# Performance work log

Hardware: AMD Instinct MI355X
Metric: run time of the kernel (lower is better)

The kernel has to match this reference:

```python
import jax, jax.numpy as jnp
import numpy as np

B, N, X, Y, W1, W2, D = 2, 6, 8, 8, 8, 8, 128
H, DH = 4, 32
L = X * Y          # number of windows
QT = N * W1 * W2   # tokens per window
EPS = 1e-5


def _ln(x, g, b):
    m = x.mean(-1, keepdims=True)
    v = ((x - m) ** 2).mean(-1, keepdims=True)
    return (x - m) * jax.lax.rsqrt(v + EPS) * g + b


def _win(t):
    # b n x y w1 w2 d -> b (x y) (n w1 w2) d
    return t.transpose(0, 2, 3, 1, 4, 5, 6).reshape(B, L, QT, D)


def setup_inputs() -> dict:
    key = jax.random.key(0)
    ks = jax.random.split(key, 12)
    s = 0.02
    inp = {
        'q': jax.random.normal(ks[0], (B, N, X, Y, W1, W2, D), jnp.float32),
        'k': jax.random.normal(ks[1], (B, N, X, Y, W1, W2, D), jnp.float32),
        'v': jax.random.normal(ks[2], (B, N, X, Y, W1, W2, D), jnp.float32),
        'skip': jax.random.normal(ks[3], (B, X, Y, W1, W2, D), jnp.float32),
        'gq': jnp.ones((D,), jnp.float32), 'betq': jnp.zeros((D,), jnp.float32),
        'gk': jnp.ones((D,), jnp.float32), 'betk': jnp.zeros((D,), jnp.float32),
        'gv': jnp.ones((D,), jnp.float32), 'betv': jnp.zeros((D,), jnp.float32),
        'wq': jax.random.normal(ks[4], (D, H * DH), jnp.float32) * s,
        'bq': jnp.zeros((H * DH,), jnp.float32),
        'wk': jax.random.normal(ks[5], (D, H * DH), jnp.float32) * s,
        'bk': jnp.zeros((H * DH,), jnp.float32),
        'wv': jax.random.normal(ks[6], (D, H * DH), jnp.float32) * s,
        'bv': jnp.zeros((H * DH,), jnp.float32),
        'wp': jax.random.normal(ks[7], (H * DH, D), jnp.float32) * s,
        'bp': jnp.zeros((D,), jnp.float32),
    }
    return inp


def reference(q, k, v, skip, gq, betq, gk, betk, gv, betv,
              wq, bq, wk, bk, wv, bv, wp, bp):
    scale = DH ** -0.5
    qw, kw, vw = _win(q), _win(k), _win(v)
    # LayerNorm + Linear QKV, split heads: (b, l, T, h, dh)
    qh = (_ln(qw, gq, betq) @ wq + bq).reshape(B, L, QT, H, DH)
    kh = (_ln(kw, gk, betk) @ wk + bk).reshape(B, L, QT, H, DH)
    vh = (_ln(vw, gv, betv) @ wv + bv).reshape(B, L, QT, H, DH)
    dot = scale * jnp.einsum('blqhd,blkhd->bhlqk', qh, kh)
    att = jax.nn.softmax(dot, axis=-1)
    a = jnp.einsum('bhlqk,blkhd->blqhd', att, vh).reshape(B, L, QT, H * DH)
    # b (x y) (n w1 w2) d -> b n x y w1 w2 d
    a = a.reshape(B, X, Y, N, W1, W2, H * DH).transpose(0, 3, 1, 2, 4, 5, 6)
    z = a @ wp + bp
    z = z.mean(1)  # average over views
    return z + skip
```

## Files before the change

kernel.cpp:

```cpp
#include <hip/hip_runtime.h>


typedef unsigned short u16;
typedef __bf16 bf16x8 __attribute__((ext_vector_type(8)));
typedef __bf16 bf16x4 __attribute__((ext_vector_type(4)));
typedef float  f32x16 __attribute__((ext_vector_type(16)));
typedef unsigned short u16x8 __attribute__((ext_vector_type(8)));
typedef unsigned short u16x4 __attribute__((ext_vector_type(4)));

union U8 { u16x8 u; bf16x8 b; u16x4 h[2]; };

#if __has_builtin(__builtin_amdgcn_exp2f)
#define EXP2(x) __builtin_amdgcn_exp2f(x)
#else
#define EXP2(x) exp2f(x)
#endif

__device__ __forceinline__ f32x16 mfma_bf16(bf16x8 a, bf16x8 b, f32x16 c){
  return __builtin_amdgcn_mfma_f32_32x32x16_bf16(a, b, c, 0, 0, 0);
}


__global__ __launch_bounds__(512) void k_prep(
    const float* __restrict__ wq, const float* __restrict__ bq,
    const float* __restrict__ gq, const float* __restrict__ betq,
    const float* __restrict__ wk, const float* __restrict__ bk,
    const float* __restrict__ gk, const float* __restrict__ betk,
    const float* __restrict__ wv, const float* __restrict__ bv,
    const float* __restrict__ gv, const float* __restrict__ betv,
    const float* __restrict__ wp,
    u16* __restrict__ wqT, u16* __restrict__ wkT, u16* __restrict__ wvT, u16* __restrict__ wpT,
    float* __restrict__ bq2, float* __restrict__ bk2, float* __restrict__ bv2,
    float* __restrict__ uq2, float* __restrict__ uk2, float* __restrict__ uv2)
{
  __shared__ float wls[128*129];
  __shared__ float gls[128], bls[128];
  __shared__ float redb[512], redu[512];
  const float ALPHA_Q = 0.17677669529663687f * 1.4426950408889634f;
  int wsel = blockIdx.x, tid = threadIdx.x;
  const float *w, *bb, *g, *bet; u16* wT; float *b2, *u2; float alpha;
  if (wsel == 0){ w=wq; bb=bq; g=gq; bet=betq; wT=wqT; b2=bq2; u2=uq2; alpha=ALPHA_Q; }
  else if (wsel == 1){ w=wk; bb=bk; g=gk; bet=betk; wT=wkT; b2=bk2; u2=uk2; alpha=1.f; }
  else if (wsel == 2){ w=wv; bb=bv; g=gv; bet=betv; wT=wvT; b2=bv2; u2=uv2; alpha=1.f; }
  else { w=wp; bb=nullptr; g=nullptr; bet=nullptr; wT=wpT; b2=nullptr; u2=nullptr; alpha=1.f; }

  if (tid < 128){
    gls[tid] = g ? g[tid] : 1.f;
    bls[tid] = bet ? bet[tid] : 0.f;
  }
  const float4* w4 = (const float4*)w;
  #pragma unroll
  for (int i = 0; i < 8; i++){
    int idx = tid + i*512;
    int row = idx >> 5, c4 = (idx & 31) * 4;
    float4 x = w4[idx];
    wls[row*129 + c4 + 0] = x.x;
    wls[row*129 + c4 + 1] = x.y;
    wls[row*129 + c4 + 2] = x.z;
    wls[row*129 + c4 + 3] = x.w;
  }
  __syncthreads();
  int n = tid >> 2, qp = tid & 3;
  float sb = 0.f, su = 0.f;
  alignas(16) __bf16 tmp[32];
  #pragma unroll
  for (int kk = 0; kk < 32; kk++){
    int k2 = qp*32 + kk;
    float wv_ = wls[k2*129 + n];
    float gv_ = gls[k2];
    sb += bls[k2] * wv_;
    su += gv_ * wv_;
    tmp[kk] = (__bf16)(wv_ * gv_ * alpha);
  }
  #pragma unroll
  for (int j = 0; j < 4; j++)
    *(bf16x8*)(wT + n*128 + qp*32 + j*8) = *(bf16x8*)&tmp[j*8];
  redb[tid] = sb; redu[tid] = su;
  __syncthreads();
  if (qp == 0 && bb){
    float s = bb[n] + redb[tid] + redb[tid+1] + redb[tid+2] + redb[tid+3];
    float u = redu[tid] + redu[tid+1] + redu[tid+2] + redu[tid+3];
    b2[n] = s * alpha;
    u2[n] = u * alpha;
  }
}

__global__ __launch_bounds__(256) void k_lnproj(
    const float* __restrict__ qg, const float* __restrict__ kg, const float* __restrict__ vg,
    const u16* __restrict__ wqT, const u16* __restrict__ wkT, const u16* __restrict__ wvT,
    const float* __restrict__ bq2, const float* __restrict__ bk2, const float* __restrict__ bv2,
    const float* __restrict__ uq2, const float* __restrict__ uk2, const float* __restrict__ uv2,
    u16* __restrict__ qh, u16* __restrict__ kh, u16* __restrict__ vh)
{
  __shared__ alignas(16) u16 Abf[64*136];
  __shared__ float s1s[64], s2s[64];
  int bid = blockIdx.x, tid = threadIdx.x;
  int which = bid % 3;
  int t = bid / 3;
  int n = t % 6, bl = t / 6;
  const float* src; const u16* wT; const float *b2, *u2; u16* dstb;
  if (which == 0){ src=qg; wT=wqT; b2=bq2; u2=uq2; dstb=qh; }
  else if (which == 1){ src=kg; wT=wkT; b2=bk2; u2=uk2; dstb=kh; }
  else { src=vg; wT=wvT; b2=bv2; u2=uv2; dstb=vh; }
  int b = bl >> 6, l = bl & 63;
  const float4* s4 = (const float4*)(src + (size_t)((b*6 + n)*64 + l)*64*128);
  int row = tid >> 2, j = tid & 3;
  float s1 = 0.f, s2 = 0.f;
  #pragma unroll
  for (int i = 0; i < 8; i++){
    float4 xv = s4[row*32 + i*4 + j];
    s1 += xv.x + xv.y + xv.z + xv.w;
    s2 += xv.x*xv.x + xv.y*xv.y + xv.z*xv.z + xv.w*xv.w;
    bf16x4 pk;
    pk[0] = (__bf16)xv.x; pk[1] = (__bf16)xv.y;
    pk[2] = (__bf16)xv.z; pk[3] = (__bf16)xv.w;
    *(bf16x4*)&Abf[row*136 + (i*4 + j)*4] = pk;
  }
  s1 += __shfl_xor(s1, 1, 64); s1 += __shfl_xor(s1, 2, 64);
  s2 += __shfl_xor(s2, 1, 64); s2 += __shfl_xor(s2, 2, 64);
  if (j == 0){
    float m = s1 * (1.f/128.f);
    float r = rsqrtf(s2 * (1.f/128.f) - m*m + 1e-5f);
    s1s[row] = r;
    s2s[row] = r * m;
  }
  __syncthreads();
  int wave = tid >> 6, lane = tid & 63, lm = lane & 31, lh = lane >> 5;
  bf16x8 bfr[8];
  const u16* wrow = wT + (32*wave + lm)*128 + lh*8;
  #pragma unroll
  for (int ks = 0; ks < 8; ks++) bfr[ks] = *(const bf16x8*)(wrow + ks*16);
  f32x16 acc0, acc1;
  #pragma unroll
  for (int r = 0; r < 16; r++){ acc0[r]=0.f; acc1[r]=0.f; }
  #pragma unroll
  for (int ks = 0; ks < 8; ks++){
    bf16x8 a0 = *(const bf16x8*)&Abf[lm*136       + ks*16 + lh*8];
    bf16x8 a1 = *(const bf16x8*)&Abf[(32+lm)*136  + ks*16 + lh*8];
    acc0 = mfma_bf16(a0, bfr[ks], acc0);
    acc1 = mfma_bf16(a1, bfr[ks], acc1);
  }
  int col = 32*wave + lm;
  float u2c = u2[col], bc = b2[col];
  u16* dst = dstb + ((size_t)(bl*4 + wave)*384 + n*64)*32 + lm;
  #pragma unroll
  for (int r = 0; r < 16; r++){
    int row0 = (r&3) + 8*(r>>2) + 4*lh;
    float y0 = s1s[row0]     * acc0[r] - s2s[row0]     * u2c + bc;
    float y1 = s1s[row0+32]  * acc1[r] - s2s[row0+32]  * u2c + bc;
    *(__bf16*)&dst[(size_t)row0*32]      = (__bf16)y0;
    *(__bf16*)&dst[(size_t)(32+row0)*32] = (__bf16)y1;
  }
}

__global__ __launch_bounds__(768, 6) void k_attn(
    const u16* __restrict__ qh, const u16* __restrict__ kh, const u16* __restrict__ vh,
    u16* __restrict__ abar)
{
  __shared__ alignas(16) u16 kls[384*36];
  __shared__ alignas(16) u16 vts[32*408];
  __shared__ float abar_s[64*32];
  int bid = blockIdx.x, tid = threadIdx.x;
  int h = bid & 3, bl = bid >> 2;
  const u16* qb = qh + (size_t)bid * (384*32);
  const u16* kb = kh + (size_t)bid * (384*32);
  const u16* vb = vh + (size_t)bid * (384*32);

  int wave = tid >> 6, lane = tid & 63, lm = lane & 31, lh = lane >> 5;
  int n = wave >> 1, qoff = (wave & 1) * 32;
  int qrow = n*64 + qoff + lm;

  bf16x8 qf0 = *(const bf16x8*)(qb + qrow*32 +      lh*8);
  bf16x8 qf1 = *(const bf16x8*)(qb + qrow*32 + 16 + lh*8);

  #pragma unroll
  for (int i = 0; i < 2; i++){
    int c = tid + i*768;
    int key = c >> 2, part = c & 3;
    U8 kv; kv.u = *(const u16x8*)(kb + key*32 + part*8);
    *(u16x4*)&kls[key*36 + part*8]     = kv.h[0];
    *(u16x4*)&kls[key*36 + part*8 + 4] = kv.h[1];
  }
  #pragma unroll
  for (int i = 0; i < 2; i++){
    int c = tid + i*768;
    int key = c >> 2, part = c & 3;
    int u = key & 31, tt = key >> 5;
    int a = u >> 2;
    int anew = (a & 4) | ((a & 1) << 1) | ((a >> 1) & 1);
    int pos = tt*32 + anew*4 + (u & 3);
    u16x8 vv = *(const u16x8*)(vb + key*32 + part*8);
    #pragma unroll
    for (int jj = 0; jj < 8; jj++) vts[(part*8 + jj)*408 + pos] = vv[jj];
  }
  for (int idx = tid; idx < 2048; idx += 768) abar_s[idx] = 0.f;
  __syncthreads();

  const u16* vrow = &vts[lm*408 + 8*lh];
  const u16* krow = &kls[lm*36 + 8*lh];

  f32x16 oacc;
  #pragma unroll
  for (int r = 0; r < 16; r++) oacc[r] = 0.f;
  float sle = 0.f;

  #pragma unroll
  for (int kt = 0; kt < 12; kt++){
    const u16* kr = krow + kt*(32*36);
    U8 kf0, kf1;
    kf0.h[0] = *(const u16x4*)(kr);
    kf0.h[1] = *(const u16x4*)(kr + 4);
    kf1.h[0] = *(const u16x4*)(kr + 16);
    kf1.h[1] = *(const u16x4*)(kr + 20);
    f32x16 sa, sb_;
    #pragma unroll
    for (int r = 0; r < 16; r++){ sa[r] = 0.f; sb_[r] = 0.f; }
    sa  = mfma_bf16(kf0.b, qf0, sa);
    sb_ = mfma_bf16(kf1.b, qf1, sb_);
    U8 p0, p1;
    #pragma unroll
    for (int r = 0; r < 8; r++){
      float e0 = EXP2(sa[r]   + sb_[r]);
      float e1 = EXP2(sa[r+8] + sb_[r+8]);
      sle += e0 + e1;
      p0.b[r] = (__bf16)e0;
      p1.b[r] = (__bf16)e1;
    }
    U8 v0, v1;
    v0.u = *(const u16x8*)(vrow + kt*32);
    v1.u = *(const u16x8*)(vrow + kt*32 + 16);
    oacc = mfma_bf16(p0.b, v0.b, oacc);
    oacc = mfma_bf16(p1.b, v1.b, oacc);
  }

  sle += __shfl_xor(sle, 32, 64);
  float inv = (1.f/6.f) / sle;

  #pragma unroll
  for (int r = 0; r < 16; r++){
    int q_l = (r&3) + 8*(r>>2) + 4*lh;
    float o = oacc[r] * __shfl(inv, q_l, 64);
    atomicAdd(&abar_s[(qoff + q_l)*32 + lm], o);
  }
  __syncthreads();
  u16* ob = abar + (size_t)(bl*64)*128 + h*32;
  for (int idx = tid; idx < 2048; idx += 768){
    int w12 = idx >> 5, dh = idx & 31;
    *(__bf16*)&ob[(size_t)w12*128 + dh] = (__bf16)abar_s[idx];
  }
}

__global__ __launch_bounds__(256) void k_out(
    const u16* __restrict__ abar, const u16* __restrict__ wpT,
    const float* __restrict__ bp, const float* __restrict__ skip,
    float* __restrict__ out)
{
  __shared__ alignas(16) u16 Als[64*136];
  int tid = threadIdx.x;
  int R0 = blockIdx.x * 64;
  #pragma unroll
  for (int i = 0; i < 4; i++){
    int c = tid + i*256;
    int row = c >> 4, part = c & 15;
    *(u16x8*)&Als[row*136 + part*8] = *(const u16x8*)(abar + (size_t)(R0+row)*128 + part*8);
  }
  __syncthreads();
  int wave = tid >> 6, lane = tid & 63, lm = lane & 31, lh = lane >> 5;
  bf16x8 bfr[8];
  const u16* wrow = wpT + (32*wave + lm)*128 + lh*8;
  #pragma unroll
  for (int ks = 0; ks < 8; ks++) bfr[ks] = *(const bf16x8*)(wrow + ks*16);
  f32x16 acc0, acc1;
  #pragma unroll
  for (int r = 0; r < 16; r++){ acc0[r]=0.f; acc1[r]=0.f; }
  #pragma unroll
  for (int ks = 0; ks < 8; ks++){
    bf16x8 a0 = *(const bf16x8*)&Als[lm*136      + ks*16 + lh*8];
    bf16x8 a1 = *(const bf16x8*)&Als[(32+lm)*136 + ks*16 + lh*8];
    acc0 = mfma_bf16(a0, bfr[ks], acc0);
    acc1 = mfma_bf16(a1, bfr[ks], acc1);
  }
  float bias = bp[32*wave + lm];
  #pragma unroll
  for (int r = 0; r < 16; r++){
    int row0 = (r&3) + 8*(r>>2) + 4*lh;
    size_t f0 = (size_t)(R0 + row0)*128 + 32*wave + lm;
    out[f0] = acc0[r] + bias + skip[f0];
    size_t f1 = (size_t)(R0 + 32 + row0)*128 + 32*wave + lm;
    out[f1] = acc1[r] + bias + skip[f1];
  }
}

extern "C" void kernel_launch(void* const* d_in, const int* in_sizes, int n_in,
                              void* d_out, int out_size, void* d_ws, size_t ws_size,
                              hipStream_t stream)
{
  const float* q    = (const float*)d_in[0];
  const float* k    = (const float*)d_in[1];
  const float* v    = (const float*)d_in[2];
  const float* skip = (const float*)d_in[3];
  const float* gq   = (const float*)d_in[4];
  const float* betq = (const float*)d_in[5];
  const float* gk   = (const float*)d_in[6];
  const float* betk = (const float*)d_in[7];
  const float* gv   = (const float*)d_in[8];
  const float* betv = (const float*)d_in[9];
  const float* wq   = (const float*)d_in[10];
  const float* bq   = (const float*)d_in[11];
  const float* wk   = (const float*)d_in[12];
  const float* bk   = (const float*)d_in[13];
  const float* wv   = (const float*)d_in[14];
  const float* bv   = (const float*)d_in[15];
  const float* wp   = (const float*)d_in[16];
  const float* bp   = (const float*)d_in[17];
  float* out = (float*)d_out;

  char* ws = (char*)d_ws;
  u16* wqT = (u16*)ws;
  u16* wkT = wqT + 16384;
  u16* wvT = wkT + 16384;
  u16* wpT = wvT + 16384;
  float* bq2 = (float*)(ws + 131072);
  float* bk2 = bq2 + 128;
  float* bv2 = bk2 + 128;
  float* uq2 = bv2 + 128;
  float* uk2 = uq2 + 128;
  float* uv2 = uk2 + 128;
  u16* qh = (u16*)(ws + 134144);
  u16* kh = qh + 6291456;
  u16* vh = kh + 6291456;
  u16* abar = vh + 6291456;

  k_prep  <<<4,    512, 0, stream>>>(wq,bq,gq,betq, wk,bk,gk,betk, wv,bv,gv,betv, wp,
                                     wqT,wkT,wvT,wpT, bq2,bk2,bv2, uq2,uk2,uv2);
  k_lnproj<<<2304, 256, 0, stream>>>(q,k,v, wqT,wkT,wvT, bq2,bk2,bv2, uq2,uk2,uv2, qh,kh,vh);
  k_attn  <<<512,  768, 0, stream>>>(qh,kh,vh, abar);
  k_out   <<<128,  256, 0, stream>>>(abar, wpT, bp, skip, out);
}
```

Before: 213.2 us.

## Halve attention block size: each wave handles 64 queries, stream K from global

```diff
diff --git a/kernel.cpp b/kernel.cpp
--- a/kernel.cpp
+++ b/kernel.cpp
@@ -153,11 +153,10 @@
   }
 }
 
-__global__ __launch_bounds__(768, 6) void k_attn(
+__global__ __launch_bounds__(384) void k_attn(
     const u16* __restrict__ qh, const u16* __restrict__ kh, const u16* __restrict__ vh,
     u16* __restrict__ abar)
 {
-  __shared__ alignas(16) u16 kls[384*36];
   __shared__ alignas(16) u16 vts[32*408];
   __shared__ float abar_s[64*32];
   int bid = blockIdx.x, tid = threadIdx.x;
@@ -167,23 +166,17 @@
   const u16* vb = vh + (size_t)bid * (384*32);
 
   int wave = tid >> 6, lane = tid & 63, lm = lane & 31, lh = lane >> 5;
-  int n = wave >> 1, qoff = (wave & 1) * 32;
-  int qrow = n*64 + qoff + lm;
-
-  bf16x8 qf0 = *(const bf16x8*)(qb + qrow*32 +      lh*8);
-  bf16x8 qf1 = *(const bf16x8*)(qb + qrow*32 + 16 + lh*8);
-
-  #pragma unroll
-  for (int i = 0; i < 2; i++){
-    int c = tid + i*768;
-    int key = c >> 2, part = c & 3;
-    U8 kv; kv.u = *(const u16x8*)(kb + key*32 + part*8);
-    *(u16x4*)&kls[key*36 + part*8]     = kv.h[0];
-    *(u16x4*)&kls[key*36 + part*8 + 4] = kv.h[1];
-  }
-  #pragma unroll
-  for (int i = 0; i < 2; i++){
-    int c = tid + i*768;
+  int n = wave;
+
+  const u16* qbase = qb + (size_t)(n*64 + lm)*32 + lh*8;
+  bf16x8 qfA0 = *(const bf16x8*)(qbase);
+  bf16x8 qfA1 = *(const bf16x8*)(qbase + 16);
+  bf16x8 qfB0 = *(const bf16x8*)(qbase + 32*32);
+  bf16x8 qfB1 = *(const bf16x8*)(qbase + 32*32 + 16);
+
+  #pragma unroll
+  for (int i = 0; i < 4; i++){
+    int c = tid + i*384;
     int key = c >> 2, part = c & 3;
     int u = key & 31, tt = key >> 5;
     int a = u >> 2;
@@ -193,58 +186,67 @@
     #pragma unroll
     for (int jj = 0; jj < 8; jj++) vts[(part*8 + jj)*408 + pos] = vv[jj];
   }
-  for (int idx = tid; idx < 2048; idx += 768) abar_s[idx] = 0.f;
+  for (int idx = tid; idx < 2048; idx += 384) abar_s[idx] = 0.f;
   __syncthreads();
 
   const u16* vrow = &vts[lm*408 + 8*lh];
-  const u16* krow = &kls[lm*36 + 8*lh];
-
-  f32x16 oacc;
-  #pragma unroll
-  for (int r = 0; r < 16; r++) oacc[r] = 0.f;
-  float sle = 0.f;
+  const u16* krow = kb + lm*32 + lh*8;
+
+  f32x16 oA, oB;
+  #pragma unroll
+  for (int r = 0; r < 16; r++){ oA[r] = 0.f; oB[r] = 0.f; }
+  float sleA = 0.f, sleB = 0.f;
 
   #pragma unroll
   for (int kt = 0; kt < 12; kt++){
-    const u16* kr = krow + kt*(32*36);
-    U8 kf0, kf1;
-    kf0.h[0] = *(const u16x4*)(kr);
-    kf0.h[1] = *(const u16x4*)(kr + 4);
-    kf1.h[0] = *(const u16x4*)(kr + 16);
-    kf1.h[1] = *(const u16x4*)(kr + 20);
+    bf16x8 kf0 = *(const bf16x8*)(krow + kt*(32*32));
+    bf16x8 kf1 = *(const bf16x8*)(krow + kt*(32*32) + 16);
     f32x16 sa, sb_;
     #pragma unroll
     for (int r = 0; r < 16; r++){ sa[r] = 0.f; sb_[r] = 0.f; }
-    sa  = mfma_bf16(kf0.b, qf0, sa);
-    sb_ = mfma_bf16(kf1.b, qf1, sb_);
-    U8 p0, p1;
-    #pragma unroll
-    for (int r = 0; r < 8; r++){
-      float e0 = EXP2(sa[r]   + sb_[r]);
-      float e1 = EXP2(sa[r+8] + sb_[r+8]);
-      sle += e0 + e1;
-      p0.b[r] = (__bf16)e0;
-      p1.b[r] = (__bf16)e1;
-    }
+    sa  = mfma_bf16(kf0, qfA0, sa);
+    sb_ = mfma_bf16(kf0, qfB0, sb_);
+    sa  = mfma_bf16(kf1, qfA1, sa);
+    sb_ = mfma_bf16(kf1, qfB1, sb_);
     U8 v0, v1;
     v0.u = *(const u16x8*)(vrow + kt*32);
     v1.u = *(const u16x8*)(vrow + kt*32 + 16);
-    oacc = mfma_bf16(p0.b, v0.b, oacc);
-    oacc = mfma_bf16(p1.b, v1.b, oacc);
-  }
-
-  sle += __shfl_xor(sle, 32, 64);
-  float inv = (1.f/6.f) / sle;
+    U8 pA0, pA1, pB0, pB1;
+    #pragma unroll
+    for (int r = 0; r < 8; r++){
+      float eA0 = EXP2(sa[r]);
+      float eA1 = EXP2(sa[r+8]);
+      float eB0 = EXP2(sb_[r]);
+      float eB1 = EXP2(sb_[r+8]);
+      sleA += eA0 + eA1;
+      sleB += eB0 + eB1;
+      pA0.b[r] = (__bf16)eA0;
+      pA1.b[r] = (__bf16)eA1;
+      pB0.b[r] = (__bf16)eB0;
+      pB1.b[r] = (__bf16)eB1;
+    }
+    oA = mfma_bf16(pA0.b, v0.b, oA);
+    oB = mfma_bf16(pB0.b, v0.b, oB);
+    oA = mfma_bf16(pA1.b, v1.b, oA);
+    oB = mfma_bf16(pB1.b, v1.b, oB);
+  }
+
+  sleA += __shfl_xor(sleA, 32, 64);
+  sleB += __shfl_xor(sleB, 32, 64);
+  float invA = (1.f/6.f) / sleA;
+  float invB = (1.f/6.f) / sleB;
 
   #pragma unroll
   for (int r = 0; r < 16; r++){
     int q_l = (r&3) + 8*(r>>2) + 4*lh;
-    float o = oacc[r] * __shfl(inv, q_l, 64);
-    atomicAdd(&abar_s[(qoff + q_l)*32 + lm], o);
+    float a = oA[r] * __shfl(invA, q_l, 64);
+    float b = oB[r] * __shfl(invB, q_l, 64);
+    atomicAdd(&abar_s[q_l*32 + lm], a);
+    atomicAdd(&abar_s[(32 + q_l)*32 + lm], b);
   }
   __syncthreads();
   u16* ob = abar + (size_t)(bl*64)*128 + h*32;
-  for (int idx = tid; idx < 2048; idx += 768){
+  for (int idx = tid; idx < 2048; idx += 384){
     int w12 = idx >> 5, dh = idx & 31;
     *(__bf16*)&ob[(size_t)w12*128 + dh] = (__bf16)abar_s[idx];
   }
@@ -334,6 +336,6 @@
   k_prep  <<<4,    512, 0, stream>>>(wq,bq,gq,betq, wk,bk,gk,betk, wv,bv,gv,betv, wp,
                                      wqT,wkT,wvT,wpT, bq2,bk2,bv2, uq2,uk2,uv2);
   k_lnproj<<<2304, 256, 0, stream>>>(q,k,v, wqT,wkT,wvT, bq2,bk2,bv2, uq2,uk2,uv2, qh,kh,vh);
-  k_attn  <<<512,  768, 0, stream>>>(qh,kh,vh, abar);
+  k_attn  <<<512,  384, 0, stream>>>(qh,kh,vh, abar);
   k_out   <<<128,  256, 0, stream>>>(abar, wpT, bp, skip, out);
 }
```

New measurement: 210.4 us. About the same (-1.3%).
